# Kernel tuning notes

Measured on AMD Instinct MI355X. Metric: run time of the kernel, lower is better.

The kernel has to match this reference:

```python
import jax, jax.numpy as jnp
import numpy as np

B, N, H = 16, 1024, 4
CH = (64, 128, 256, 512)
KV = 960
EPS = 1e-5  # InstanceNorm2d default eps


def setup_inputs() -> dict:
    key = jax.random.key(0)
    ks = jax.random.split(key, 16)
    s = 0.02
    inp = {
        "emb1": jax.random.normal(ks[0], (B, N, CH[0]), jnp.float32),
        "emb2": jax.random.normal(ks[1], (B, N, CH[1]), jnp.float32),
        "emb3": jax.random.normal(ks[2], (B, N, CH[2]), jnp.float32),
        "emb4": jax.random.normal(ks[3], (B, N, CH[3]), jnp.float32),
        "emb_all": jax.random.normal(ks[4], (B, N, KV), jnp.float32),
        # per-head query weights (torch Linear weight layout [out, in])
        "Wq1": jax.random.normal(ks[5], (H, CH[0] // 4, CH[0] // 4), jnp.float32) * s,
        "Wq2": jax.random.normal(ks[6], (H, CH[1] // 4, CH[1] // 4), jnp.float32) * s,
        "Wq3": jax.random.normal(ks[7], (H, CH[2] // 4, CH[2] // 4), jnp.float32) * s,
        "Wq4": jax.random.normal(ks[8], (H, CH[3] // 4, CH[3] // 4), jnp.float32) * s,
        # NOTE: original forward only ever uses self.key[0] / self.value[0]
        "Wk": jax.random.normal(ks[9], (KV // 4, KV // 4), jnp.float32) * s,
        "Wv": jax.random.normal(ks[10], (KV // 4, KV // 4), jnp.float32) * s,
        "Wo1": jax.random.normal(ks[11], (CH[0], CH[0]), jnp.float32) * s,
        "Wo2": jax.random.normal(ks[12], (CH[1], CH[1]), jnp.float32) * s,
        "Wo3": jax.random.normal(ks[13], (CH[2], CH[2]), jnp.float32) * s,
        "Wo4": jax.random.normal(ks[14], (CH[3], CH[3]), jnp.float32) * s,
    }
    return inp


def _heads_from_all(x):
    # Reproduce the per-head channel regrouping of emb_all:
    # head h takes [16h:16(h+1)] of scale1, [32h:...] of scale2, etc. -> [B,H,N,240]
    b, n, _ = x.shape
    parts = [
        x[:, :, 0:64].reshape(b, n, H, 16),
        x[:, :, 64:192].reshape(b, n, H, 32),
        x[:, :, 192:448].reshape(b, n, H, 64),
        x[:, :, 448:960].reshape(b, n, H, 128),
    ]
    return jnp.concatenate(parts, axis=-1).transpose(0, 2, 1, 3)


def _scale_attn(emb, Wq, Wo, Kh, Vh):
    b, n, c = emb.shape
    d = c // H
    q = emb.reshape(b, n, H, d)
    # per-head linear (torch: x @ W.T): [B,H,N,d]
    Qh = jnp.einsum('bnhd,hed->bhne', q, Wq)
    # channel attention: Q^T K -> [B,H,d,240]
    scores = jnp.einsum('bhnd,bhnk->bhdk', Qh, Kh) / np.float32(np.sqrt(KV))
    # InstanceNorm2d over heads (per (b,h), normalize over last two dims, biased var)
    m = scores.mean(axis=(2, 3), keepdims=True)
    v = scores.var(axis=(2, 3), keepdims=True)
    probs = jax.nn.softmax((scores - m) / jnp.sqrt(v + EPS), axis=-1)
    # probs @ V^T -> [B,H,d,N]
    ctx = jnp.einsum('bhdk,bhnk->bhdn', probs, Vh)
    # permute(0,3,2,1) -> [B,N,d,H], flatten -> [B,N,c]
    ctx = ctx.transpose(0, 3, 2, 1).reshape(b, n, c)
    return jnp.einsum('bnc,ec->bne', ctx, Wo)


def reference(emb1, emb2, emb3, emb4, emb_all,
              Wq1, Wq2, Wq3, Wq4, Wk, Wv, Wo1, Wo2, Wo3, Wo4):
    heads = _heads_from_all(emb_all)  # [B,H,N,240]
    Kh = jnp.einsum('bhnd,ed->bhne', heads, Wk)
    Vh = jnp.einsum('bhnd,ed->bhne', heads, Wv)
    O1 = _scale_attn(emb1, Wq1, Wo1, Kh, Vh)
    O2 = _scale_attn(emb2, Wq2, Wo2, Kh, Vh)
    O3 = _scale_attn(emb3, Wq3, Wo3, Kh, Vh)
    O4 = _scale_attn(emb4, Wq4, Wo4, Kh, Vh)
    return (O1, O2, O3, O4)
```

## Files before the change

kernel.cpp:

```cpp
#include <hip/hip_runtime.h>
#include <hip/hip_bf16.h>
#include <math.h>

#define B_   16
#define N_   1024
#define H_   4
#define D240 240

typedef unsigned short ushort;
typedef __attribute__((ext_vector_type(8))) short bf16x8;
typedef __attribute__((ext_vector_type(8))) unsigned short u16x8;
typedef __attribute__((ext_vector_type(4))) float f32x4;

__device__ __forceinline__ ushort f2b(float v) {
  __hip_bfloat16 h = __float2bfloat16(v);
  return *reinterpret_cast<ushort*>(&h);
}

__device__ __forceinline__ u16x8 cvt8(float4 a, float4 b) {
  u16x8 w;
  w[0] = f2b(a.x); w[1] = f2b(a.y); w[2] = f2b(a.z); w[3] = f2b(a.w);
  w[4] = f2b(b.x); w[5] = f2b(b.y); w[6] = f2b(b.z); w[7] = f2b(b.w);
  return w;
}

__device__ __forceinline__ void gload16(const void* g, void* s) {
  __builtin_amdgcn_global_load_lds((const __attribute__((address_space(1))) void*)g,
                                   (__attribute__((address_space(3))) void*)s, 16, 0, 0);
}

__device__ __forceinline__ const float* heads_src(const float* __restrict__ emb_all,
                                                  int b, int n, int h, int k) {
  int soff;
  if (k < 16)       soff = h * 16 + k;
  else if (k < 48)  soff = 64  + h * 32  + (k - 16);
  else if (k < 112) soff = 192 + h * 64  + (k - 48);
  else              soff = 448 + h * 128 + (k - 112);
  return emb_all + ((long)b * N_ + n) * 960 + soff;
}

__device__ __forceinline__ const float* emb_src(const float* __restrict__ e1,
                                                const float* __restrict__ e2,
                                                const float* __restrict__ e3,
                                                const float* __restrict__ e4,
                                                int b, int n, int h, int k, int* stride) {
  if (k < 16)  { *stride = 64;  return e1 + ((long)b * N_ + n) * 64  + h * 16  + k; }
  if (k < 48)  { *stride = 128; return e2 + ((long)b * N_ + n) * 128 + h * 32  + (k - 16); }
  if (k < 112) { *stride = 256; return e3 + ((long)b * N_ + n) * 256 + h * 64  + (k - 48); }
  *stride = 512; return e4 + ((long)b * N_ + n) * 512 + h * 128 + (k - 112);
}

__global__ __launch_bounds__(256) void conv_weights(
    const float* __restrict__ Wk, const float* __restrict__ Wv,
    const float* __restrict__ q1, const float* __restrict__ q2,
    const float* __restrict__ q3, const float* __restrict__ q4,
    const float* __restrict__ o1, const float* __restrict__ o2,
    const float* __restrict__ o3, const float* __restrict__ o4,
    ushort* __restrict__ wts) {
  long i = (long)blockIdx.x * 256 + threadIdx.x;
  if (i >= 716800) return;
  float v = 0.f;
  if (i < 122880) {
    const float* src = (i < 61440) ? Wk : Wv;
    long j = (i < 61440) ? i : i - 61440;
    int r = j / 256, k = j % 256;
    if (k < 240) v = src[(long)r * 240 + k];
  } else if (i < 368640) {
    long j = i - 122880;
    int h = j / 61440; int rem = j % 61440;
    int r = rem / 256, k = rem % 256;
    int s = r < 16 ? 0 : r < 48 ? 1 : r < 112 ? 2 : 3;
    const int dss[4] = {16, 32, 64, 128};
    const int qf[4]  = {0, 16, 48, 112};
    const float* qs[4] = {q1, q2, q3, q4};
    int d = dss[s], off = qf[s];
    if (k >= off && k < off + d)
      v = qs[s][((long)(h * d + (r - off))) * d + (k - off)];
  } else {
    long j = i - 368640;
    int s = j < 4096 ? 0 : j < 20480 ? 1 : j < 86016 ? 2 : 3;
    const long base[4] = {0, 4096, 20480, 86016};
    const int cs[4] = {64, 128, 256, 512};
    const float* os[4] = {o1, o2, o3, o4};
    long rem = j - base[s];
    int c = cs[s], d = c >> 2;
    int e = rem / c, kk = rem % c;
    v = os[s][(long)e * c + (kk % d) * 4 + kk / d];
  }
  wts[i] = f2b(v);
}

__device__ __forceinline__ void core_w_g(
    ushort* As, ushort* Bs,
    const ushort* __restrict__ Aw, long lda, int M,
    const float* __restrict__ emb_all,
    const float* __restrict__ e1, const float* __restrict__ e2,
    const float* __restrict__ e3, const float* __restrict__ e4,
    int gmode, int b, int h,
    ushort* __restrict__ C, long ldc, int m0, int n0, int K)
{
  const int tid = threadIdx.x;
  const int l = tid & 63, w = tid >> 6;
  const int wy = w >> 1, wx = w & 1;

  f32x4 acc[4][4];
  #pragma unroll
  for (int i = 0; i < 4; ++i)
    #pragma unroll
    for (int j = 0; j < 4; ++j) acc[i][j] = (f32x4)0.f;

  const int srow = tid >> 2;
  const int skc  = (tid & 3) * 8;
  int ra0 = m0 + srow;      ra0 = ra0 < M ? ra0 : M - 1;
  int ra1 = m0 + srow + 64; ra1 = ra1 < M ? ra1 : M - 1;
  const ushort* a0 = Aw + (long)ra0 * lda + skc;
  const ushort* a1 = Aw + (long)ra1 * lda + skc;
  ushort* lA0 = As + srow * 32 + skc;
  ushort* lA1 = As + (srow + 64) * 32 + skc;
  ushort* lB0 = Bs + srow * 32 + skc;
  ushort* lB1 = Bs + (srow + 64) * 32 + skc;
  const int nrow = n0 + srow;

  const ushort* arp = As + (wy * 64 + (l & 15)) * 32 + (l >> 4) * 8;
  const ushort* brp = Bs + (wx * 64 + (l & 15)) * 32 + (l >> 4) * 8;

  for (int k0 = 0; k0 < K; k0 += 32) {
    __syncthreads();
    gload16(a0 + k0, lA0);
    gload16(a1 + k0, lA1);
    const int k = k0 + skc;
    u16x8 w0, w1;
    if (k < 240) {
      const float* s0; int stride;
      if (gmode == 0) { stride = 960; s0 = heads_src(emb_all, b, nrow, h, k); }
      else            { s0 = emb_src(e1, e2, e3, e4, b, nrow, h, k, &stride); }
      const float* s1 = s0 + (long)64 * stride;
      float4 p0 = *(const float4*)s0, p1 = *(const float4*)(s0 + 4);
      float4 q0 = *(const float4*)s1, q1 = *(const float4*)(s1 + 4);
      w0 = cvt8(p0, p1); w1 = cvt8(q0, q1);
    } else {
      w0 = (u16x8)0; w1 = (u16x8)0;
    }
    *(u16x8*)lB0 = w0;
    *(u16x8*)lB1 = w1;
    __syncthreads();
    bf16x8 af[4], bfr[4];
    #pragma unroll
    for (int i = 0; i < 4; ++i) af[i]  = *(const bf16x8*)(arp + i * 512);
    #pragma unroll
    for (int j = 0; j < 4; ++j) bfr[j] = *(const bf16x8*)(brp + j * 512);
    #pragma unroll
    for (int i = 0; i < 4; ++i)
      #pragma unroll
      for (int j = 0; j < 4; ++j)
        acc[i][j] = __builtin_amdgcn_mfma_f32_16x16x32_bf16(af[i], bfr[j], acc[i][j], 0, 0, 0);
  }

  const int quad = l >> 4, lc = l & 15;
  #pragma unroll
  for (int i = 0; i < 4; ++i) {
    #pragma unroll
    for (int r = 0; r < 4; ++r) {
      int row = m0 + wy * 64 + i * 16 + quad * 4 + r;
      if (row >= M) continue;
      ushort* Cr = C + (long)row * ldc;
      #pragma unroll
      for (int j = 0; j < 4; ++j) {
        int col = n0 + wx * 64 + j * 16 + lc;
        Cr[col] = f2b(acc[i][j][r]);
      }
    }
  }
}

__device__ __forceinline__ void core_g_w(
    ushort* As, ushort* Bs,
    const float* __restrict__ emb_all, int b, int h,
    const ushort* __restrict__ Bw, long ldb, int Nn, int Npad,
    ushort* __restrict__ C, long ldc, int m0, int n0, int K)
{
  const int tid = threadIdx.x;
  const int l = tid & 63, w = tid >> 6;
  const int wy = w >> 1, wx = w & 1;

  f32x4 acc[4][4];
  #pragma unroll
  for (int i = 0; i < 4; ++i)
    #pragma unroll
    for (int j = 0; j < 4; ++j) acc[i][j] = (f32x4)0.f;

  const int srow = tid >> 2;
  const int skc  = (tid & 3) * 8;
  int rb0 = n0 + srow;      rb0 = rb0 < Nn ? rb0 : Nn - 1;
  int rb1 = n0 + srow + 64; rb1 = rb1 < Nn ? rb1 : Nn - 1;
  const ushort* b0 = Bw + (long)rb0 * ldb + skc;
  const ushort* b1 = Bw + (long)rb1 * ldb + skc;
  ushort* lA0 = As + srow * 32 + skc;
  ushort* lA1 = As + (srow + 64) * 32 + skc;
  ushort* lB0 = Bs + srow * 32 + skc;
  ushort* lB1 = Bs + (srow + 64) * 32 + skc;
  const int mrow = m0 + srow;

  const ushort* arp = As + (wy * 64 + (l & 15)) * 32 + (l >> 4) * 8;
  const ushort* brp = Bs + (wx * 64 + (l & 15)) * 32 + (l >> 4) * 8;

  for (int k0 = 0; k0 < K; k0 += 32) {
    __syncthreads();
    gload16(b0 + k0, lB0);
    gload16(b1 + k0, lB1);
    const int k = k0 + skc;
    u16x8 w0, w1;
    if (k < 240) {
      const float* s0 = heads_src(emb_all, b, mrow, h, k);
      const float* s1 = s0 + (long)64 * 960;
      float4 p0 = *(const float4*)s0, p1 = *(const float4*)(s0 + 4);
      float4 q0 = *(const float4*)s1, q1 = *(const float4*)(s1 + 4);
      w0 = cvt8(p0, p1); w1 = cvt8(q0, q1);
    } else {
      w0 = (u16x8)0; w1 = (u16x8)0;
    }
    *(u16x8*)lA0 = w0;
    *(u16x8*)lA1 = w1;
    __syncthreads();
    bf16x8 af[4], bfr[4];
    #pragma unroll
    for (int i = 0; i < 4; ++i) af[i]  = *(const bf16x8*)(arp + i * 512);
    #pragma unroll
    for (int j = 0; j < 4; ++j) bfr[j] = *(const bf16x8*)(brp + j * 512);
    #pragma unroll
    for (int i = 0; i < 4; ++i)
      #pragma unroll
      for (int j = 0; j < 4; ++j)
        acc[i][j] = __builtin_amdgcn_mfma_f32_16x16x32_bf16(af[i], bfr[j], acc[i][j], 0, 0, 0);
  }

  const int quad = l >> 4, lc = l & 15;
  #pragma unroll
  for (int i = 0; i < 4; ++i) {
    #pragma unroll
    for (int r = 0; r < 4; ++r) {
      int row = m0 + wy * 64 + i * 16 + quad * 4 + r;
      ushort* Cr = C + (long)row * ldc;
      #pragma unroll
      for (int j = 0; j < 4; ++j) {
        int col = n0 + wx * 64 + j * 16 + lc;
        if (col < Nn) Cr[col] = f2b(acc[i][j][r]);
        else if (col < Npad) Cr[col] = 0;
      }
    }
  }
}

__global__ __launch_bounds__(256) void mfma_proj(
    const float* __restrict__ emb_all,
    const float* __restrict__ e1, const float* __restrict__ e2,
    const float* __restrict__ e3, const float* __restrict__ e4,
    const ushort* __restrict__ Wk_b, const ushort* __restrict__ Wv_b,
    const ushort* __restrict__ Wq_bd,
    ushort* __restrict__ Kh_T, ushort* __restrict__ Vh, ushort* __restrict__ Q_T)
{
  __shared__ __align__(16) ushort As[128 * 32];
  __shared__ __align__(16) ushort Bs[128 * 32];
  const int bx = blockIdx.x;

  if (bx < 1024) {
    const int bh = bx >> 4, t = bx & 15;
    const int b = bh >> 2, h = bh & 3;
    core_w_g(As, Bs, Wk_b, 256, 240,
             emb_all, e1, e2, e3, e4, 0, b, h,
             Kh_T + (long)bh * 240 * 1024, 1024,
             (t >> 3) * 128, (t & 7) * 128, 256);
  } else if (bx < 2048) {
    const int local = bx - 1024;
    const int bh = local >> 4, t = local & 15;
    const int b = bh >> 2, h = bh & 3;
    core_g_w(As, Bs, emb_all, b, h,
             Wv_b, 256, 240, 256,
             Vh + (long)bh * 1024 * 256, 256,
             (t >> 1) * 128, (t & 1) * 128, 256);
  } else {
    const int local = bx - 2048;
    const int bh = local >> 4, t = local & 15;
    const int b = bh >> 2, h = bh & 3;
    core_w_g(As, Bs, Wq_bd + h * 61440, 256, 240,
             emb_all, e1, e2, e3, e4, 1, b, h,
             Q_T + (long)bh * 240 * 1024, 1024,
             (t >> 3) * 128, (t & 7) * 128, 256);
  }
}

__global__ __launch_bounds__(512) void fused_sm(const ushort* __restrict__ Q_T,
                                                const ushort* __restrict__ Kh_T,
                                                ushort* __restrict__ P,
                                                float alpha) {
  const int sidx = blockIdx.x, bh = blockIdx.y;
  const int dss[4]   = {16, 32, 64, 128};
  const int doffs[4] = {0, 16, 48, 112};
  const int ds = dss[sidx], doff = doffs[sidx];

  const int tid = threadIdx.x;
  const int l = tid & 63, w = tid >> 6;
  const int wy = w >> 2, wx = w & 3;

  __shared__ __align__(16) ushort As[128 * 32];
  __shared__ __align__(16) ushort Bs[256 * 32];
  __shared__ float red[2][2][64][4];
  __shared__ float wred[2][8];

  f32x4 acc[4][4];
  #pragma unroll
  for (int i = 0; i < 4; ++i)
    #pragma unroll
    for (int j = 0; j < 4; ++j) acc[i][j] = (f32x4)0.f;

  const int srow = tid >> 2;
  const int skc  = (tid & 3) * 8;
  const long qbase = (long)bh * 240 * 1024;
  int qa = doff + (srow < ds ? srow : ds - 1);
  const ushort* a0 = Q_T + qbase + (long)qa * 1024 + skc;
  int kb1 = (srow + 128) < 240 ? (srow + 128) : 239;
  const ushort* b0 = Kh_T + qbase + (long)srow * 1024 + skc;
  const ushort* b1 = Kh_T + qbase + (long)kb1 * 1024 + skc;
  ushort* lA0 = As + srow * 32 + skc;
  ushort* lB0 = Bs + srow * 32 + skc;
  ushort* lB1 = Bs + (srow + 128) * 32 + skc;

  const ushort* arp = As + (wy * 64 + (l & 15)) * 32 + (l >> 4) * 8;
  const ushort* brp = Bs + (wx * 64 + (l & 15)) * 32 + (l >> 4) * 8;

  for (int k0 = 0; k0 < 1024; k0 += 32) {
    __syncthreads();
    gload16(a0 + k0, lA0);
    gload16(b0 + k0, lB0);
    gload16(b1 + k0, lB1);
    __syncthreads();
    bf16x8 af[4], bfr[4];
    #pragma unroll
    for (int i = 0; i < 4; ++i) af[i]  = *(const bf16x8*)(arp + i * 512);
    #pragma unroll
    for (int j = 0; j < 4; ++j) bfr[j] = *(const bf16x8*)(brp + j * 512);
    #pragma unroll
    for (int i = 0; i < 4; ++i)
      #pragma unroll
      for (int j = 0; j < 4; ++j)
        acc[i][j] = __builtin_amdgcn_mfma_f32_16x16x32_bf16(af[i], bfr[j], acc[i][j], 0, 0, 0);
  }

  const int quad = l >> 4, lc = l & 15;

  float s1 = 0.f, s2 = 0.f;
  #pragma unroll
  for (int i = 0; i < 4; ++i) {
    #pragma unroll
    for (int j = 0; j < 4; ++j) {
      const int col = wx * 64 + j * 16 + lc;
      #pragma unroll
      for (int r = 0; r < 4; ++r) {
        const int rl = wy * 64 + i * 16 + quad * 4 + r;
        float v = acc[i][j][r] * alpha;
        acc[i][j][r] = v;
        if (rl < ds && col < 240) { s1 += v; s2 += v * v; }
      }
    }
  }
  #pragma unroll
  for (int o = 32; o > 0; o >>= 1) { s1 += __shfl_xor(s1, o); s2 += __shfl_xor(s2, o); }
  if (l == 0) { wred[0][w] = s1; wred[1][w] = s2; }
  __syncthreads();
  float ts = 0.f, ts2 = 0.f;
  #pragma unroll
  for (int ww = 0; ww < 8; ++ww) { ts += wred[0][ww]; ts2 += wred[1][ww]; }
  const float cnt = (float)(ds * 240);
  const float mean = ts / cnt;
  const float var = ts2 / cnt - mean * mean;
  const float rstd = rsqrtf(var + 1e-5f);

  float rmax[4][4];
  #pragma unroll
  for (int i = 0; i < 4; ++i) {
    #pragma unroll
    for (int r = 0; r < 4; ++r) {
      float m = -1e30f;
      #pragma unroll
      for (int j = 0; j < 4; ++j) {
        const int col = wx * 64 + j * 16 + lc;
        float z = (acc[i][j][r] - mean) * rstd;
        acc[i][j][r] = z;
        if (col < 240) m = fmaxf(m, z);
      }
      m = fmaxf(m, __shfl_xor(m, 1));
      m = fmaxf(m, __shfl_xor(m, 2));
      m = fmaxf(m, __shfl_xor(m, 4));
      m = fmaxf(m, __shfl_xor(m, 8));
      rmax[i][r] = m;
    }
  }
  if (lc == 0) {
    #pragma unroll
    for (int i = 0; i < 4; ++i)
      #pragma unroll
      for (int r = 0; r < 4; ++r)
        red[0][wy][i * 16 + quad * 4 + r][wx] = rmax[i][r];
  }
  __syncthreads();
  #pragma unroll
  for (int i = 0; i < 4; ++i) {
    #pragma unroll
    for (int r = 0; r < 4; ++r) {
      const int rl = i * 16 + quad * 4 + r;
      float m = red[0][wy][rl][0];
      m = fmaxf(m, red[0][wy][rl][1]);
      m = fmaxf(m, red[0][wy][rl][2]);
      m = fmaxf(m, red[0][wy][rl][3]);
      rmax[i][r] = m;
    }
  }

  float rsum[4][4];
  #pragma unroll
  for (int i = 0; i < 4; ++i) {
    #pragma unroll
    for (int r = 0; r < 4; ++r) {
      float sacc = 0.f;
      #pragma unroll
      for (int j = 0; j < 4; ++j) {
        const int col = wx * 64 + j * 16 + lc;
        float e = (col < 240) ? __expf(acc[i][j][r] - rmax[i][r]) : 0.f;
        acc[i][j][r] = e;
        sacc += e;
      }
      sacc += __shfl_xor(sacc, 1);
      sacc += __shfl_xor(sacc, 2);
      sacc += __shfl_xor(sacc, 4);
      sacc += __shfl_xor(sacc, 8);
      rsum[i][r] = sacc;
    }
  }
  if (lc == 0) {
    #pragma unroll
    for (int i = 0; i < 4; ++i)
      #pragma unroll
      for (int r = 0; r < 4; ++r)
        red[1][wy][i * 16 + quad * 4 + r][wx] = rsum[i][r];
  }
  __syncthreads();

  #pragma unroll
  for (int i = 0; i < 4; ++i) {
    #pragma unroll
    for (int r = 0; r < 4; ++r) {
      const int rl = wy * 64 + i * 16 + quad * 4 + r;
      if (rl >= ds) continue;
      const int rli = i * 16 + quad * 4 + r;
      float tot = red[1][wy][rli][0] + red[1][wy][rli][1] +
                  red[1][wy][rli][2] + red[1][wy][rli][3];
      float inv = 1.f / tot;
      ushort* Pr = P + ((long)bh * 240 + doff + rl) * 256;
      #pragma unroll
      for (int j = 0; j < 4; ++j) {
        const int col = wx * 64 + j * 16 + lc;
        Pr[col] = (col < 240) ? f2b(acc[i][j][r] * inv) : (ushort)0;
      }
    }
  }
}

__global__ __launch_bounds__(256) void mfma_ctx(const ushort* __restrict__ V,
                                                const ushort* __restrict__ P,
                                                ushort* __restrict__ ctx2) {
  const int h = blockIdx.y, b = blockIdx.z;
  const ushort* A  = V + (((long)b * H_ + h) * 1024) * 256;
  const ushort* Bm = P + (((long)b * H_ + h) * 240) * 256;

  const int m0 = (blockIdx.x >> 1) * 128;
  const int n0 = (blockIdx.x & 1) * 128;
  const int tid = threadIdx.x;
  const int l = tid & 63, w = tid >> 6;
  const int wy = w >> 1, wx = w & 1;

  __shared__ __align__(16) ushort As[128 * 32];
  __shared__ __align__(16) ushort Bs[128 * 32];

  f32x4 acc[4][4];
  #pragma unroll
  for (int i = 0; i < 4; ++i)
    #pragma unroll
    for (int j = 0; j < 4; ++j) acc[i][j] = (f32x4)0.f;

  const int srow = tid >> 2;
  const int skc  = (tid & 3) * 8;
  int rb0 = n0 + srow;      rb0 = rb0 < 240 ? rb0 : 239;
  int rb1 = n0 + srow + 64; rb1 = rb1 < 240 ? rb1 : 239;
  const ushort* a0 = A  + (long)(m0 + srow) * 256 + skc;
  const ushort* a1 = A  + (long)(m0 + srow + 64) * 256 + skc;
  const ushort* b0 = Bm + (long)rb0 * 256 + skc;
  const ushort* b1 = Bm + (long)rb1 * 256 + skc;
  ushort* lA0 = As + srow * 32 + skc;
  ushort* lA1 = As + (srow + 64) * 32 + skc;
  ushort* lB0 = Bs + srow * 32 + skc;
  ushort* lB1 = Bs + (srow + 64) * 32 + skc;

  const ushort* arp = As + (wy * 64 + (l & 15)) * 32 + (l >> 4) * 8;
  const ushort* brp = Bs + (wx * 64 + (l & 15)) * 32 + (l >> 4) * 8;

  for (int k0 = 0; k0 < 256; k0 += 32) {
    __syncthreads();
    gload16(a0 + k0, lA0);
    gload16(a1 + k0, lA1);
    gload16(b0 + k0, lB0);
    gload16(b1 + k0, lB1);
    __syncthreads();
    bf16x8 af[4], bfr[4];
    #pragma unroll
    for (int i = 0; i < 4; ++i) af[i]  = *(const bf16x8*)(arp + i * 512);
    #pragma unroll
    for (int j = 0; j < 4; ++j) bfr[j] = *(const bf16x8*)(brp + j * 512);
    #pragma unroll
    for (int i = 0; i < 4; ++i)
      #pragma unroll
      for (int j = 0; j < 4; ++j)
        acc[i][j] = __builtin_amdgcn_mfma_f32_16x16x32_bf16(af[i], bfr[j], acc[i][j], 0, 0, 0);
  }

  const int quad = l >> 4, lc = l & 15;
  const int dss[4] = {16, 32, 64, 128};
  const int qf[4]  = {0, 16, 48, 112};
  const int cf[4]  = {0, 64, 192, 448};
  #pragma unroll
  for (int i = 0; i < 4; ++i) {
    #pragma unroll
    for (int r = 0; r < 4; ++r) {
      int row = m0 + wy * 64 + i * 16 + quad * 4 + r;
      ushort* Cr = ctx2 + ((long)b * N_ + row) * 960;
      #pragma unroll
      for (int j = 0; j < 4; ++j) {
        int col = n0 + wx * 64 + j * 16 + lc;
        if (col < 240) {
          int s = col < 16 ? 0 : col < 48 ? 1 : col < 112 ? 2 : 3;
          int chan = cf[s] + h * dss[s] + (col - qf[s]);
          Cr[chan] = f2b(acc[i][j][r]);
        }
      }
    }
  }
}

__global__ __launch_bounds__(256) void mfma_oproj(const ushort* __restrict__ ctx2,
                                                  const ushort* __restrict__ Wo_b,
                                                  float* __restrict__ out) {
  const int bx = blockIdx.x;
  int s = bx < 128 ? 0 : bx < 256 ? 1 : bx < 512 ? 2 : 3;
  const int sbase[4] = {0, 128, 256, 512};
  const int cs_[4]   = {64, 128, 256, 512};
  const int coff_[4] = {0, 64, 192, 448};
  const int wo_[4]   = {0, 4096, 20480, 86016};
  const long oo_[4]  = {0, 1048576, 3145728, 7340032};
  const int c = cs_[s];
  const int nt = (c + 127) >> 7;
  const int local = bx - sbase[s];
  const int m0 = (local / nt) * 128;
  const int n0 = (local % nt) * 128;

  const ushort* A  = ctx2 + coff_[s];
  const ushort* Bm = Wo_b + wo_[s];
  float* C = out + oo_[s];
  const int K = c, Nn = c;

  const int tid = threadIdx.x;
  const int l = tid & 63, w = tid >> 6;
  const int wy = w >> 1, wx = w & 1;

  __shared__ __align__(16) ushort As[128 * 32];
  __shared__ __align__(16) ushort Bs[128 * 32];

  f32x4 acc[4][4];
  #pragma unroll
  for (int i = 0; i < 4; ++i)
    #pragma unroll
    for (int j = 0; j < 4; ++j) acc[i][j] = (f32x4)0.f;

  const int srow = tid >> 2;
  const int skc  = (tid & 3) * 8;
  int rb0 = n0 + srow;      rb0 = rb0 < Nn ? rb0 : Nn - 1;
  int rb1 = n0 + srow + 64; rb1 = rb1 < Nn ? rb1 : Nn - 1;
  const ushort* a0 = A  + (long)(m0 + srow) * 960 + skc;
  const ushort* a1 = A  + (long)(m0 + srow + 64) * 960 + skc;
  const ushort* b0 = Bm + (long)rb0 * c + skc;
  const ushort* b1 = Bm + (long)rb1 * c + skc;
  ushort* lA0 = As + srow * 32 + skc;
  ushort* lA1 = As + (srow + 64) * 32 + skc;
  ushort* lB0 = Bs + srow * 32 + skc;
  ushort* lB1 = Bs + (srow + 64) * 32 + skc;

  const ushort* arp = As + (wy * 64 + (l & 15)) * 32 + (l >> 4) * 8;
  const ushort* brp = Bs + (wx * 64 + (l & 15)) * 32 + (l >> 4) * 8;

  for (int k0 = 0; k0 < K; k0 += 32) {
    __syncthreads();
    gload16(a0 + k0, lA0);
    gload16(a1 + k0, lA1);
    gload16(b0 + k0, lB0);
    gload16(b1 + k0, lB1);
    __syncthreads();
    bf16x8 af[4], bfr[4];
    #pragma unroll
    for (int i = 0; i < 4; ++i) af[i]  = *(const bf16x8*)(arp + i * 512);
    #pragma unroll
    for (int j = 0; j < 4; ++j) bfr[j] = *(const bf16x8*)(brp + j * 512);
    #pragma unroll
    for (int i = 0; i < 4; ++i)
      #pragma unroll
      for (int j = 0; j < 4; ++j)
        acc[i][j] = __builtin_amdgcn_mfma_f32_16x16x32_bf16(af[i], bfr[j], acc[i][j], 0, 0, 0);
  }

  const int quad = l >> 4, lc = l & 15;
  #pragma unroll
  for (int i = 0; i < 4; ++i) {
    #pragma unroll
    for (int r = 0; r < 4; ++r) {
      int row = m0 + wy * 64 + i * 16 + quad * 4 + r;
      float* Cr = C + (long)row * c;
      #pragma unroll
      for (int j = 0; j < 4; ++j) {
        int col = n0 + wx * 64 + j * 16 + lc;
        if (col < Nn) Cr[col] = acc[i][j][r];
      }
    }
  }
}

extern "C" void kernel_launch(void* const* d_in, const int* in_sizes, int n_in,
                              void* d_out, int out_size, void* d_ws, size_t ws_size,
                              hipStream_t stream) {
  const float* emb[4] = {(const float*)d_in[0], (const float*)d_in[1],
                         (const float*)d_in[2], (const float*)d_in[3]};
  const float* emb_all = (const float*)d_in[4];
  const float* Wq[4] = {(const float*)d_in[5], (const float*)d_in[6],
                        (const float*)d_in[7], (const float*)d_in[8]};
  const float* Wk = (const float*)d_in[9];
  const float* Wv = (const float*)d_in[10];
  const float* Wo[4] = {(const float*)d_in[11], (const float*)d_in[12],
                        (const float*)d_in[13], (const float*)d_in[14]};
  float* out = (float*)d_out;

  ushort* wsb     = (ushort*)d_ws;
  ushort* ctx2    = wsb;
  ushort* P_b     = wsb + 16777216;
  ushort* Q_T     = wsb + 33554432;
  ushort* Kh_T    = wsb + 49283072;
  ushort* Vh      = wsb + 65011712;
  ushort* wts     = wsb + 81788928;
  ushort* Wk_b  = wts;
  ushort* Wv_b  = wts + 61440;
  ushort* Wq_bd = wts + 122880;
  ushort* Wo_b  = wts + 368640;

  const float alpha_s = 1.0f / sqrtf(960.0f);

  conv_weights<<<dim3(2800), 256, 0, stream>>>(Wk, Wv, Wq[0], Wq[1], Wq[2], Wq[3],
                                               Wo[0], Wo[1], Wo[2], Wo[3], wts);

  mfma_proj<<<dim3(3072), 256, 0, stream>>>(emb_all, emb[0], emb[1], emb[2], emb[3],
                                            Wk_b, Wv_b, Wq_bd, Kh_T, Vh, Q_T);

  fused_sm<<<dim3(4, 64), 512, 0, stream>>>(Q_T, Kh_T, P_b, alpha_s);

  mfma_ctx<<<dim3(16, H_, B_), 256, 0, stream>>>(Vh, P_b, ctx2);

  mfma_oproj<<<dim3(1024), 256, 0, stream>>>(ctx2, Wo_b, out);
}
```

Measured before the change: 345.8 us.

## Double-buffer LDS tiles in projection GEMM cores to overlap loads with MFMA

Both projection GEMM cores now use two LDS buffers. The next K-tile's weight and fp32 activation loads are issued before the current tile's MFMA work, and the converted activations are written to the other buffer afterwards. This drops one barrier per iteration and hides global-load latency behind compute. In exchange, shared memory per block doubles and more registers are held across the MFMA section, which may reduce occupancy.

```diff
diff --git a/kernel.cpp b/kernel.cpp
--- a/kernel.cpp
+++ b/kernel.cpp
@@ -90,6 +90,8 @@
   wts[i] = f2b(v);
 }
 
+#define BUFSZ 4096
+
 __device__ __forceinline__ void core_w_g(
     ushort* As, ushort* Bs,
     const ushort* __restrict__ Aw, long lda, int M,
@@ -124,36 +126,62 @@
   const ushort* arp = As + (wy * 64 + (l & 15)) * 32 + (l >> 4) * 8;
   const ushort* brp = Bs + (wx * 64 + (l & 15)) * 32 + (l >> 4) * 8;
 
-  for (int k0 = 0; k0 < K; k0 += 32) {
-    __syncthreads();
-    gload16(a0 + k0, lA0);
-    gload16(a1 + k0, lA1);
-    const int k = k0 + skc;
+  gload16(a0, lA0);
+  gload16(a1, lA1);
+  {
+    const int k = skc;
     u16x8 w0, w1;
     if (k < 240) {
       const float* s0; int stride;
       if (gmode == 0) { stride = 960; s0 = heads_src(emb_all, b, nrow, h, k); }
       else            { s0 = emb_src(e1, e2, e3, e4, b, nrow, h, k, &stride); }
       const float* s1 = s0 + (long)64 * stride;
-      float4 p0 = *(const float4*)s0, p1 = *(const float4*)(s0 + 4);
-      float4 q0 = *(const float4*)s1, q1 = *(const float4*)(s1 + 4);
-      w0 = cvt8(p0, p1); w1 = cvt8(q0, q1);
-    } else {
-      w0 = (u16x8)0; w1 = (u16x8)0;
-    }
+      w0 = cvt8(*(const float4*)s0, *(const float4*)(s0 + 4));
+      w1 = cvt8(*(const float4*)s1, *(const float4*)(s1 + 4));
+    } else { w0 = (u16x8)0; w1 = (u16x8)0; }
     *(u16x8*)lB0 = w0;
     *(u16x8*)lB1 = w1;
-    __syncthreads();
+  }
+  __syncthreads();
+
+  const int nt = K >> 5;
+  for (int t = 0; t < nt; ++t) {
+    const int cur = (t & 1) * BUFSZ;
+    const int nxt = cur ^ BUFSZ;
+    const bool have = (t + 1) < nt;
+    const int kn = (t + 1) * 32 + skc;
+    const bool doload = have && (kn < 240);
+    float4 p0, p1, q0, q1;
+    if (have) {
+      gload16(a0 + (t + 1) * 32, lA0 + nxt);
+      gload16(a1 + (t + 1) * 32, lA1 + nxt);
+    }
+    if (doload) {
+      const float* s0; int stride;
+      if (gmode == 0) { stride = 960; s0 = heads_src(emb_all, b, nrow, h, kn); }
+      else            { s0 = emb_src(e1, e2, e3, e4, b, nrow, h, kn, &stride); }
+      const float* s1 = s0 + (long)64 * stride;
+      p0 = *(const float4*)s0; p1 = *(const float4*)(s0 + 4);
+      q0 = *(const float4*)s1; q1 = *(const float4*)(s1 + 4);
+    }
     bf16x8 af[4], bfr[4];
     #pragma unroll
-    for (int i = 0; i < 4; ++i) af[i]  = *(const bf16x8*)(arp + i * 512);
-    #pragma unroll
-    for (int j = 0; j < 4; ++j) bfr[j] = *(const bf16x8*)(brp + j * 512);
+    for (int i = 0; i < 4; ++i) af[i]  = *(const bf16x8*)(arp + cur + i * 512);
+    #pragma unroll
+    for (int j = 0; j < 4; ++j) bfr[j] = *(const bf16x8*)(brp + cur + j * 512);
     #pragma unroll
     for (int i = 0; i < 4; ++i)
       #pragma unroll
       for (int j = 0; j < 4; ++j)
         acc[i][j] = __builtin_amdgcn_mfma_f32_16x16x32_bf16(af[i], bfr[j], acc[i][j], 0, 0, 0);
+    if (have) {
+      u16x8 w0, w1;
+      if (doload) { w0 = cvt8(p0, p1); w1 = cvt8(q0, q1); }
+      else        { w0 = (u16x8)0; w1 = (u16x8)0; }
+      *(u16x8*)(lB0 + nxt) = w0;
+      *(u16x8*)(lB1 + nxt) = w1;
+    }
+    __syncthreads();
   }
 
   const int quad = l >> 4, lc = l & 15;
@@ -204,34 +232,58 @@
   const ushort* arp = As + (wy * 64 + (l & 15)) * 32 + (l >> 4) * 8;
   const ushort* brp = Bs + (wx * 64 + (l & 15)) * 32 + (l >> 4) * 8;
 
-  for (int k0 = 0; k0 < K; k0 += 32) {
-    __syncthreads();
-    gload16(b0 + k0, lB0);
-    gload16(b1 + k0, lB1);
-    const int k = k0 + skc;
+  gload16(b0, lB0);
+  gload16(b1, lB1);
+  {
+    const int k = skc;
     u16x8 w0, w1;
     if (k < 240) {
       const float* s0 = heads_src(emb_all, b, mrow, h, k);
       const float* s1 = s0 + (long)64 * 960;
-      float4 p0 = *(const float4*)s0, p1 = *(const float4*)(s0 + 4);
-      float4 q0 = *(const float4*)s1, q1 = *(const float4*)(s1 + 4);
-      w0 = cvt8(p0, p1); w1 = cvt8(q0, q1);
-    } else {
-      w0 = (u16x8)0; w1 = (u16x8)0;
-    }
+      w0 = cvt8(*(const float4*)s0, *(const float4*)(s0 + 4));
+      w1 = cvt8(*(const float4*)s1, *(const float4*)(s1 + 4));
+    } else { w0 = (u16x8)0; w1 = (u16x8)0; }
     *(u16x8*)lA0 = w0;
     *(u16x8*)lA1 = w1;
-    __syncthreads();
+  }
+  __syncthreads();
+
+  const int nt = K >> 5;
+  for (int t = 0; t < nt; ++t) {
+    const int cur = (t & 1) * BUFSZ;
+    const int nxt = cur ^ BUFSZ;
+    const bool have = (t + 1) < nt;
+    const int kn = (t + 1) * 32 + skc;
+    const bool doload = have && (kn < 240);
+    float4 p0, p1, q0, q1;
+    if (have) {
+      gload16(b0 + (t + 1) * 32, lB0 + nxt);
+      gload16(b1 + (t + 1) * 32, lB1 + nxt);
+    }
+    if (doload) {
+      const float* s0 = heads_src(emb_all, b, mrow, h, kn);
+      const float* s1 = s0 + (long)64 * 960;
+      p0 = *(const float4*)s0; p1 = *(const float4*)(s0 + 4);
+      q0 = *(const float4*)s1; q1 = *(const float4*)(s1 + 4);
+    }
     bf16x8 af[4], bfr[4];
     #pragma unroll
-    for (int i = 0; i < 4; ++i) af[i]  = *(const bf16x8*)(arp + i * 512);
-    #pragma unroll
-    for (int j = 0; j < 4; ++j) bfr[j] = *(const bf16x8*)(brp + j * 512);
+    for (int i = 0; i < 4; ++i) af[i]  = *(const bf16x8*)(arp + cur + i * 512);
+    #pragma unroll
+    for (int j = 0; j < 4; ++j) bfr[j] = *(const bf16x8*)(brp + cur + j * 512);
     #pragma unroll
     for (int i = 0; i < 4; ++i)
       #pragma unroll
       for (int j = 0; j < 4; ++j)
         acc[i][j] = __builtin_amdgcn_mfma_f32_16x16x32_bf16(af[i], bfr[j], acc[i][j], 0, 0, 0);
+    if (have) {
+      u16x8 w0, w1;
+      if (doload) { w0 = cvt8(p0, p1); w1 = cvt8(q0, q1); }
+      else        { w0 = (u16x8)0; w1 = (u16x8)0; }
+      *(u16x8*)(lA0 + nxt) = w0;
+      *(u16x8*)(lA1 + nxt) = w1;
+    }
+    __syncthreads();
   }
 
   const int quad = l >> 4, lc = l & 15;
@@ -259,8 +311,8 @@
     const ushort* __restrict__ Wq_bd,
     ushort* __restrict__ Kh_T, ushort* __restrict__ Vh, ushort* __restrict__ Q_T)
 {
-  __shared__ __align__(16) ushort As[128 * 32];
-  __shared__ __align__(16) ushort Bs[128 * 32];
+  __shared__ __align__(16) ushort As[2 * 128 * 32];
+  __shared__ __align__(16) ushort Bs[2 * 128 * 32];
   const int bx = blockIdx.x;
 
   if (bx < 1024) {
```

Result: slower. 357.7 us (+3.4%).

## Load projection GEMM operands directly into registers, dropping LDS staging

Applied to the files above, without the earlier changes.

The projection kernel's GEMM cores no longer stage A and B tiles through shared memory with barriers. Each lane now loads its MFMA fragments straight from global memory: the bf16 weights as 16-byte loads and the fp32 activations converted to bf16 on the fly, with the K loop fully unrolled. This removes the LDS writes and reads and the two __syncthreads per K step. In exchange, data is no longer shared across waves, so each wave re-reads operands from global memory or cache and issues more and less coalesced loads, and register pressure rises.

```diff
diff --git a/kernel.cpp b/kernel.cpp
--- a/kernel.cpp
+++ b/kernel.cpp
@@ -17,37 +17,16 @@
   return *reinterpret_cast<ushort*>(&h);
 }
 
-__device__ __forceinline__ u16x8 cvt8(float4 a, float4 b) {
+__device__ __forceinline__ bf16x8 cvt8b(float4 a, float4 b) {
   u16x8 w;
   w[0] = f2b(a.x); w[1] = f2b(a.y); w[2] = f2b(a.z); w[3] = f2b(a.w);
   w[4] = f2b(b.x); w[5] = f2b(b.y); w[6] = f2b(b.z); w[7] = f2b(b.w);
-  return w;
+  return *reinterpret_cast<bf16x8*>(&w);
 }
 
 __device__ __forceinline__ void gload16(const void* g, void* s) {
   __builtin_amdgcn_global_load_lds((const __attribute__((address_space(1))) void*)g,
                                    (__attribute__((address_space(3))) void*)s, 16, 0, 0);
-}
-
-__device__ __forceinline__ const float* heads_src(const float* __restrict__ emb_all,
-                                                  int b, int n, int h, int k) {
-  int soff;
-  if (k < 16)       soff = h * 16 + k;
-  else if (k < 48)  soff = 64  + h * 32  + (k - 16);
-  else if (k < 112) soff = 192 + h * 64  + (k - 48);
-  else              soff = 448 + h * 128 + (k - 112);
-  return emb_all + ((long)b * N_ + n) * 960 + soff;
-}
-
-__device__ __forceinline__ const float* emb_src(const float* __restrict__ e1,
-                                                const float* __restrict__ e2,
-                                                const float* __restrict__ e3,
-                                                const float* __restrict__ e4,
-                                                int b, int n, int h, int k, int* stride) {
-  if (k < 16)  { *stride = 64;  return e1 + ((long)b * N_ + n) * 64  + h * 16  + k; }
-  if (k < 48)  { *stride = 128; return e2 + ((long)b * N_ + n) * 128 + h * 32  + (k - 16); }
-  if (k < 112) { *stride = 256; return e3 + ((long)b * N_ + n) * 256 + h * 64  + (k - 48); }
-  *stride = 512; return e4 + ((long)b * N_ + n) * 512 + h * 128 + (k - 112);
 }
 
 __global__ __launch_bounds__(256) void conv_weights(
@@ -90,18 +69,18 @@
   wts[i] = f2b(v);
 }
 
-__device__ __forceinline__ void core_w_g(
-    ushort* As, ushort* Bs,
-    const ushort* __restrict__ Aw, long lda, int M,
+__device__ __forceinline__ void proj_wg_direct(
+    const ushort* __restrict__ Aw, int M,
     const float* __restrict__ emb_all,
     const float* __restrict__ e1, const float* __restrict__ e2,
     const float* __restrict__ e3, const float* __restrict__ e4,
     int gmode, int b, int h,
-    ushort* __restrict__ C, long ldc, int m0, int n0, int K)
+    ushort* __restrict__ C, long ldc, int m0, int n0)
 {
   const int tid = threadIdx.x;
   const int l = tid & 63, w = tid >> 6;
   const int wy = w >> 1, wx = w & 1;
+  const int kq = (l >> 4) * 8;
 
   f32x4 acc[4][4];
   #pragma unroll
@@ -109,46 +88,49 @@
     #pragma unroll
     for (int j = 0; j < 4; ++j) acc[i][j] = (f32x4)0.f;
 
-  const int srow = tid >> 2;
-  const int skc  = (tid & 3) * 8;
-  int ra0 = m0 + srow;      ra0 = ra0 < M ? ra0 : M - 1;
-  int ra1 = m0 + srow + 64; ra1 = ra1 < M ? ra1 : M - 1;
-  const ushort* a0 = Aw + (long)ra0 * lda + skc;
-  const ushort* a1 = Aw + (long)ra1 * lda + skc;
-  ushort* lA0 = As + srow * 32 + skc;
-  ushort* lA1 = As + (srow + 64) * 32 + skc;
-  ushort* lB0 = Bs + srow * 32 + skc;
-  ushort* lB1 = Bs + (srow + 64) * 32 + skc;
-  const int nrow = n0 + srow;
-
-  const ushort* arp = As + (wy * 64 + (l & 15)) * 32 + (l >> 4) * 8;
-  const ushort* brp = Bs + (wx * 64 + (l & 15)) * 32 + (l >> 4) * 8;
-
-  for (int k0 = 0; k0 < K; k0 += 32) {
-    __syncthreads();
-    gload16(a0 + k0, lA0);
-    gload16(a1 + k0, lA1);
-    const int k = k0 + skc;
-    u16x8 w0, w1;
-    if (k < 240) {
-      const float* s0; int stride;
-      if (gmode == 0) { stride = 960; s0 = heads_src(emb_all, b, nrow, h, k); }
-      else            { s0 = emb_src(e1, e2, e3, e4, b, nrow, h, k, &stride); }
-      const float* s1 = s0 + (long)64 * stride;
-      float4 p0 = *(const float4*)s0, p1 = *(const float4*)(s0 + 4);
-      float4 q0 = *(const float4*)s1, q1 = *(const float4*)(s1 + 4);
-      w0 = cvt8(p0, p1); w1 = cvt8(q0, q1);
+  const ushort* ap[4];
+  #pragma unroll
+  for (int i = 0; i < 4; ++i) {
+    int r = m0 + wy * 64 + i * 16 + (l & 15);
+    r = r < M ? r : M - 1;
+    ap[i] = Aw + (long)r * 256 + kq;
+  }
+  long rbn[4];
+  #pragma unroll
+  for (int j = 0; j < 4; ++j) {
+    int n = n0 + wx * 64 + j * 16 + (l & 15);
+    rbn[j] = (long)b * N_ + n;
+  }
+
+  #pragma unroll
+  for (int k0 = 0; k0 < 256; k0 += 32) {
+    const int kk = k0 + kq;
+    bf16x8 af[4], bfr[4];
+    #pragma unroll
+    for (int i = 0; i < 4; ++i) af[i] = *(const bf16x8*)(ap[i] + k0);
+    if (kk < 240) {
+      #pragma unroll
+      for (int j = 0; j < 4; ++j) {
+        const float* s;
+        if (gmode == 0) {
+          int soff;
+          if (kk < 16)       soff = h * 16 + kk;
+          else if (kk < 48)  soff = 64  + h * 32  + (kk - 16);
+          else if (kk < 112) soff = 192 + h * 64  + (kk - 48);
+          else               soff = 448 + h * 128 + (kk - 112);
+          s = emb_all + rbn[j] * 960 + soff;
+        } else {
+          if (kk < 16)       s = e1 + rbn[j] * 64  + h * 16  + kk;
+          else if (kk < 48)  s = e2 + rbn[j] * 128 + h * 32  + (kk - 16);
+          else if (kk < 112) s = e3 + rbn[j] * 256 + h * 64  + (kk - 48);
+          else               s = e4 + rbn[j] * 512 + h * 128 + (kk - 112);
+        }
+        bfr[j] = cvt8b(*(const float4*)s, *(const float4*)(s + 4));
+      }
     } else {
-      w0 = (u16x8)0; w1 = (u16x8)0;
-    }
-    *(u16x8*)lB0 = w0;
-    *(u16x8*)lB1 = w1;
-    __syncthreads();
-    bf16x8 af[4], bfr[4];
-    #pragma unroll
-    for (int i = 0; i < 4; ++i) af[i]  = *(const bf16x8*)(arp + i * 512);
-    #pragma unroll
-    for (int j = 0; j < 4; ++j) bfr[j] = *(const bf16x8*)(brp + j * 512);
+      #pragma unroll
+      for (int j = 0; j < 4; ++j) bfr[j] = (bf16x8)(short)0;
+    }
     #pragma unroll
     for (int i = 0; i < 4; ++i)
       #pragma unroll
@@ -173,15 +155,15 @@
   }
 }
 
-__device__ __forceinline__ void core_g_w(
-    ushort* As, ushort* Bs,
+__device__ __forceinline__ void proj_gw_direct(
     const float* __restrict__ emb_all, int b, int h,
-    const ushort* __restrict__ Bw, long ldb, int Nn, int Npad,
-    ushort* __restrict__ C, long ldc, int m0, int n0, int K)
+    const ushort* __restrict__ Bw, int Nn, int Npad,
+    ushort* __restrict__ C, long ldc, int m0, int n0)
 {
   const int tid = threadIdx.x;
   const int l = tid & 63, w = tid >> 6;
   const int wy = w >> 1, wx = w & 1;
+  const int kq = (l >> 4) * 8;
 
   f32x4 acc[4][4];
   #pragma unroll
@@ -189,44 +171,41 @@
     #pragma unroll
     for (int j = 0; j < 4; ++j) acc[i][j] = (f32x4)0.f;
 
-  const int srow = tid >> 2;
-  const int skc  = (tid & 3) * 8;
-  int rb0 = n0 + srow;      rb0 = rb0 < Nn ? rb0 : Nn - 1;
-  int rb1 = n0 + srow + 64; rb1 = rb1 < Nn ? rb1 : Nn - 1;
-  const ushort* b0 = Bw + (long)rb0 * ldb + skc;
-  const ushort* b1 = Bw + (long)rb1 * ldb + skc;
-  ushort* lA0 = As + srow * 32 + skc;
-  ushort* lA1 = As + (srow + 64) * 32 + skc;
-  ushort* lB0 = Bs + srow * 32 + skc;
-  ushort* lB1 = Bs + (srow + 64) * 32 + skc;
-  const int mrow = m0 + srow;
-
-  const ushort* arp = As + (wy * 64 + (l & 15)) * 32 + (l >> 4) * 8;
-  const ushort* brp = Bs + (wx * 64 + (l & 15)) * 32 + (l >> 4) * 8;
-
-  for (int k0 = 0; k0 < K; k0 += 32) {
-    __syncthreads();
-    gload16(b0 + k0, lB0);
-    gload16(b1 + k0, lB1);
-    const int k = k0 + skc;
-    u16x8 w0, w1;
-    if (k < 240) {
-      const float* s0 = heads_src(emb_all, b, mrow, h, k);
-      const float* s1 = s0 + (long)64 * 960;
-      float4 p0 = *(const float4*)s0, p1 = *(const float4*)(s0 + 4);
-      float4 q0 = *(const float4*)s1, q1 = *(const float4*)(s1 + 4);
-      w0 = cvt8(p0, p1); w1 = cvt8(q0, q1);
+  long ran[4];
+  #pragma unroll
+  for (int i = 0; i < 4; ++i) {
+    int m = m0 + wy * 64 + i * 16 + (l & 15);
+    ran[i] = (long)b * N_ + m;
+  }
+  const ushort* bp[4];
+  #pragma unroll
+  for (int j = 0; j < 4; ++j) {
+    int r = n0 + wx * 64 + j * 16 + (l & 15);
+    r = r < Nn ? r : Nn - 1;
+    bp[j] = Bw + (long)r * 256 + kq;
+  }
+
+  #pragma unroll
+  for (int k0 = 0; k0 < 256; k0 += 32) {
+    const int kk = k0 + kq;
+    bf16x8 af[4], bfr[4];
+    #pragma unroll
+    for (int j = 0; j < 4; ++j) bfr[j] = *(const bf16x8*)(bp[j] + k0);
+    if (kk < 240) {
+      int soff;
+      if (kk < 16)       soff = h * 16 + kk;
+      else if (kk < 48)  soff = 64  + h * 32  + (kk - 16);
+      else if (kk < 112) soff = 192 + h * 64  + (kk - 48);
+      else               soff = 448 + h * 128 + (kk - 112);
+      #pragma unroll
+      for (int i = 0; i < 4; ++i) {
+        const float* s = emb_all + ran[i] * 960 + soff;
+        af[i] = cvt8b(*(const float4*)s, *(const float4*)(s + 4));
+      }
     } else {
-      w0 = (u16x8)0; w1 = (u16x8)0;
-    }
-    *(u16x8*)lA0 = w0;
-    *(u16x8*)lA1 = w1;
-    __syncthreads();
-    bf16x8 af[4], bfr[4];
-    #pragma unroll
-    for (int i = 0; i < 4; ++i) af[i]  = *(const bf16x8*)(arp + i * 512);
-    #pragma unroll
-    for (int j = 0; j < 4; ++j) bfr[j] = *(const bf16x8*)(brp + j * 512);
+      #pragma unroll
+      for (int i = 0; i < 4; ++i) af[i] = (bf16x8)(short)0;
+    }
     #pragma unroll
     for (int i = 0; i < 4; ++i)
       #pragma unroll
@@ -259,33 +238,31 @@
     const ushort* __restrict__ Wq_bd,
     ushort* __restrict__ Kh_T, ushort* __restrict__ Vh, ushort* __restrict__ Q_T)
 {
-  __shared__ __align__(16) ushort As[128 * 32];
-  __shared__ __align__(16) ushort Bs[128 * 32];
   const int bx = blockIdx.x;
 
   if (bx < 1024) {
     const int bh = bx >> 4, t = bx & 15;
     const int b = bh >> 2, h = bh & 3;
-    core_w_g(As, Bs, Wk_b, 256, 240,
-             emb_all, e1, e2, e3, e4, 0, b, h,
-             Kh_T + (long)bh * 240 * 1024, 1024,
-             (t >> 3) * 128, (t & 7) * 128, 256);
+    proj_wg_direct(Wk_b, 240,
+                   emb_all, e1, e2, e3, e4, 0, b, h,
+                   Kh_T + (long)bh * 240 * 1024, 1024,
+                   (t >> 3) * 128, (t & 7) * 128);
   } else if (bx < 2048) {
     const int local = bx - 1024;
     const int bh = local >> 4, t = local & 15;
     const int b = bh >> 2, h = bh & 3;
-    core_g_w(As, Bs, emb_all, b, h,
-             Wv_b, 256, 240, 256,
-             Vh + (long)bh * 1024 * 256, 256,
-             (t >> 1) * 128, (t & 1) * 128, 256);
+    proj_gw_direct(emb_all, b, h,
+                   Wv_b, 240, 256,
+                   Vh + (long)bh * 1024 * 256, 256,
+                   (t >> 1) * 128, (t & 1) * 128);
   } else {
     const int local = bx - 2048;
     const int bh = local >> 4, t = local & 15;
     const int b = bh >> 2, h = bh & 3;
-    core_w_g(As, Bs, Wq_bd + h * 61440, 256, 240,
-             emb_all, e1, e2, e3, e4, 1, b, h,
-             Q_T + (long)bh * 240 * 1024, 1024,
-             (t >> 3) * 128, (t & 7) * 128, 256);
+    proj_wg_direct(Wq_bd + h * 61440, 240,
+                   emb_all, e1, e2, e3, e4, 1, b, h,
+                   Q_T + (long)bh * 240 * 1024, 1024,
+                   (t >> 3) * 128, (t & 7) * 128);
   }
 }
 
```

New measurement: 408.6 us. 18.2% more time.
